# Optimization experiments

Measured on AMD Instinct MI355X. Metric: run time of the kernel, lower is better.

## Reference

```python
import jax, jax.numpy as jnp
import numpy as np

WS = 7      # window size
SHIFT = 3   # shift size
H = 56
W = 56
NH = 16     # num heads


def _layernorm(x, g, b):
    m = x.mean(-1, keepdims=True)
    v = x.var(-1, keepdims=True)
    return (x - m) / jnp.sqrt(v + 1e-5) * g + b


def setup_inputs() -> dict:
    key = jax.random.key(0)
    ks = jax.random.split(key, 8)
    B, C = 16, 512
    DH = 4 * C
    s = 0.02
    x = jax.random.normal(ks[0], (B, H * W, C), jnp.float32)

    # relative position index (matches torch buffer construction)
    coords = np.stack(np.meshgrid(np.arange(WS), np.arange(WS), indexing='ij')).reshape(2, -1)
    rel = (coords[:, :, None] - coords[:, None, :]).transpose(1, 2, 0).copy()
    rel[..., 0] += WS - 1
    rel[..., 1] += WS - 1
    rel[..., 0] *= 2 * WS - 1
    rpi = jnp.asarray(rel.sum(-1), jnp.int32)  # (49, 49)

    # shifted-window additive attention mask (nW, N, N)
    img = np.zeros((H, W))
    cnt = 0
    for hs in (slice(0, -WS), slice(-WS, -SHIFT), slice(-SHIFT, None)):
        for wsl in (slice(0, -WS), slice(-WS, -SHIFT), slice(-SHIFT, None)):
            img[hs, wsl] = cnt
            cnt += 1
    mw = img.reshape(H // WS, WS, W // WS, WS).transpose(0, 2, 1, 3).reshape(-1, WS * WS)
    diff = mw[:, None, :] - mw[:, :, None]  # == mw.unsqueeze(1) - mw.unsqueeze(2)
    attn_mask = jnp.asarray(np.where(diff != 0, -100.0, 0.0), jnp.float32)

    return {
        'x': x,
        'rpi': rpi,
        'attn_mask': attn_mask,
        'norm1_g': jnp.ones((C,), jnp.float32),
        'norm1_b': jnp.zeros((C,), jnp.float32),
        'qkv_w': jax.random.normal(ks[1], (3 * C, C), jnp.float32) * s,
        'qkv_b': jnp.zeros((3 * C,), jnp.float32),
        'proj_w': jax.random.normal(ks[2], (C, C), jnp.float32) * s,
        'proj_b': jnp.zeros((C,), jnp.float32),
        'rpb_table': jax.random.normal(ks[3], ((2 * WS - 1) ** 2, NH), jnp.float32) * s,
        'norm2_g': jnp.ones((C,), jnp.float32),
        'norm2_b': jnp.zeros((C,), jnp.float32),
        'mlp_w1': jax.random.normal(ks[4], (DH, C), jnp.float32) * s,
        'mlp_b1': jnp.zeros((DH,), jnp.float32),
        'mlp_w2': jax.random.normal(ks[5], (C, DH), jnp.float32) * s,
        'mlp_b2': jnp.zeros((C,), jnp.float32),
    }


def reference(x, rpi, attn_mask, norm1_g, norm1_b, qkv_w, qkv_b, proj_w, proj_b,
              rpb_table, norm2_g, norm2_b, mlp_w1, mlp_b1, mlp_w2, mlp_b2):
    B, L, C = x.shape
    N = WS * WS
    nW = (H // WS) * (W // WS)
    hd = C // NH

    # --- attention branch ---
    h = _layernorm(x, norm1_g, norm1_b).reshape(B, H, W, C)
    h = jnp.roll(h, (-SHIFT, -SHIFT), axis=(1, 2))
    # window partition -> (B*nW, N, C)
    xw = h.reshape(B, H // WS, WS, W // WS, WS, C).transpose(0, 1, 3, 2, 4, 5).reshape(B * nW, N, C)

    qkv = (xw @ qkv_w.T + qkv_b).reshape(B * nW, N, 3, NH, hd).transpose(2, 0, 3, 1, 4)
    q, k, v = qkv[0], qkv[1], qkv[2]  # (B*nW, NH, N, hd)
    attn = jnp.einsum('bhnd,bhmd->bhnm', q * (hd ** -0.5), k)
    rpb = rpb_table[rpi].transpose(2, 0, 1)  # (NH, N, N)
    attn = attn + rpb[None]
    attn = attn.reshape(B, nW, NH, N, N) + attn_mask[None, :, None]
    attn = jax.nn.softmax(attn.reshape(B * nW, NH, N, N), axis=-1)
    o = jnp.einsum('bhnm,bhmd->bhnd', attn, v).transpose(0, 2, 1, 3).reshape(B * nW, N, C)
    o = o @ proj_w.T + proj_b
    # window reverse + unshift
    o = o.reshape(B, H // WS, W // WS, WS, WS, C).transpose(0, 1, 3, 2, 4, 5).reshape(B, H, W, C)
    o = jnp.roll(o, (SHIFT, SHIFT), axis=(1, 2)).reshape(B, L, C)

    x = x + o
    # --- MLP branch ---
    h2 = _layernorm(x, norm2_g, norm2_b)
    m = jax.nn.gelu(h2 @ mlp_w1.T + mlp_b1, approximate=False)
    return x + (m @ mlp_w2.T + mlp_b2)
```

## Files before the change

### kernel.cpp

```cpp
#include <hip/hip_runtime.h>
#include <hip/hip_bf16.h>

typedef __attribute__((ext_vector_type(8))) short bf16x8_t;
typedef __attribute__((ext_vector_type(4))) float f32x4_t;

#define LD8(p) (*(const bf16x8_t*)(p))

__global__ __launch_bounds__(256) void k_cvt(const float* __restrict__ in,
                                             __hip_bfloat16* __restrict__ out, int n) {
  int i = blockIdx.x * 256 + threadIdx.x;
  if (i < n) out[i] = __float2bfloat16(in[i]);
}

__global__ __launch_bounds__(256) void k_cmb(const int* __restrict__ rpi,
                                             const float* __restrict__ tab,
                                             const float* __restrict__ mask,
                                             float* __restrict__ cmbp) {
  int idx = blockIdx.x * 256 + threadIdx.x;
  int jj = idx & 3, lane = (idx >> 2) & 63, tile = (idx >> 8) & 15;
  int h = (idx >> 12) & 15, w6 = idx >> 16;
  int r = (tile >> 2) * 16 + (lane >> 4) * 4 + jj;
  int c = (tile & 3) * 16 + (lane & 15);
  float v = -1e9f;
  if (r < 49 && c < 49) v = tab[rpi[r * 49 + c] * 16 + h] + mask[w6 * 2401 + r * 49 + c];
  cmbp[idx] = v;
}

template<int PERM>
__global__ __launch_bounds__(256) void k_ln(const float* __restrict__ in,
                                            const float* __restrict__ g,
                                            const float* __restrict__ bta,
                                            __hip_bfloat16* __restrict__ out) {
  int token = blockIdx.x;
  int t = threadIdx.x;
  const float2 v = ((const float2*)(in + (size_t)token * 512))[t];
  float s = v.x + v.y, sq = v.x * v.x + v.y * v.y;
  #pragma unroll
  for (int d = 1; d < 64; d <<= 1) { s += __shfl_xor(s, d); sq += __shfl_xor(sq, d); }
  __shared__ float ps[4], pq[4];
  int w = t >> 6;
  if ((t & 63) == 0) { ps[w] = s; pq[w] = sq; }
  __syncthreads();
  s  = ps[0] + ps[1] + ps[2] + ps[3];
  sq = pq[0] + pq[1] + pq[2] + pq[3];
  float mean = s * (1.f / 512.f);
  float inv = rsqrtf(sq * (1.f / 512.f) - mean * mean + 1e-5f);
  size_t dst;
  if (PERM) {
    int b = token / 3136, p = token - b * 3136;
    int i = p / 56, j = p - i * 56;
    int gi = (i + 53) % 56, gj = (j + 53) % 56;
    dst = ((size_t)(((b * 64) + (gi / 7) * 8 + (gj / 7)) * 49) + (gi % 7) * 7 + (gj % 7)) * 512;
  } else {
    dst = (size_t)token * 512;
  }
  int c = t * 2;
  out[dst + c]     = __float2bfloat16((v.x - mean) * inv * g[c] + bta[c]);
  out[dst + c + 1] = __float2bfloat16((v.y - mean) * inv * g[c + 1] + bta[c + 1]);
}

__global__ __launch_bounds__(256) void k_attn(const __hip_bfloat16* __restrict__ qkv,
                                              const float* __restrict__ cmbp,
                                              __hip_bfloat16* __restrict__ o) {
  __shared__ __align__(16) __hip_bfloat16 vt_all[4 * 32 * 72];
  __shared__ __align__(16) __hip_bfloat16 P_all[4 * 64 * 72];
  const int t = threadIdx.x, l = t & 63, w = t >> 6;
  const int bw = blockIdx.x;
  const int head = blockIdx.y * 4 + w;
  const int rr = l & 15, g = l >> 4;
  __hip_bfloat16* vt = vt_all + w * (32 * 72);
  __hip_bfloat16* P  = P_all  + w * (64 * 72);
  const __hip_bfloat16* base = qkv + (size_t)bw * 49 * 1536 + head * 32;
  const bf16x8_t zero8 = {};

  { int d = l >> 1, sg = (l & 1) * 8;
    *(bf16x8_t*)(vt + d * 72 + 48 + sg) = zero8; }
  __builtin_amdgcn_sched_barrier(0);
  #pragma unroll
  for (int it = 0; it < 4; ++it) {
    int idx = l + it * 64;
    if (idx < 196) {
      int j = idx >> 2, sg = (idx & 3) * 8;
      bf16x8_t vv = *(const bf16x8_t*)(base + 1024 + (size_t)j * 1536 + sg);
      #pragma unroll
      for (int s2 = 0; s2 < 8; ++s2) vt[(sg + s2) * 72 + j] = ((__hip_bfloat16*)&vv)[s2];
    }
  }
  bf16x8_t aq[4], bk[4];
  #pragma unroll
  for (int m = 0; m < 4; ++m) {
    int row = m * 16 + rr;
    aq[m] = (row < 49) ? *(const bf16x8_t*)(base + (size_t)row * 1536 + g * 8) : zero8;
    bk[m] = (row < 49) ? *(const bf16x8_t*)(base + 512 + (size_t)row * 1536 + g * 8) : zero8;
  }
  const float4* cp = (const float4*)(cmbp + (size_t)((bw & 63) * 16 + head) * 4096);
  f32x4_t S[4][4];
  #pragma unroll
  for (int tm = 0; tm < 4; ++tm)
    #pragma unroll
    for (int tn = 0; tn < 4; ++tn) {
      float4 cv = cp[(tm * 4 + tn) * 64 + l];
      f32x4_t c0 = { cv.x, cv.y, cv.z, cv.w };
      S[tm][tn] = __builtin_amdgcn_mfma_f32_16x16x32_bf16(aq[tm], bk[tn], c0, 0, 0, 0);
    }
  float sm[4][4];
  #pragma unroll
  for (int tm = 0; tm < 4; ++tm) {
    #pragma unroll
    for (int jj = 0; jj < 4; ++jj) {
      float v = fmaxf(fmaxf(S[tm][0][jj], S[tm][1][jj]), fmaxf(S[tm][2][jj], S[tm][3][jj]));
      v = fmaxf(v, __shfl_xor(v, 1));
      v = fmaxf(v, __shfl_xor(v, 2));
      v = fmaxf(v, __shfl_xor(v, 4));
      v = fmaxf(v, __shfl_xor(v, 8));
      float s = 0.f;
      #pragma unroll
      for (int tn = 0; tn < 4; ++tn) {
        float e = __expf(S[tm][tn][jj] - v);
        S[tm][tn][jj] = e;
        s += e;
      }
      s += __shfl_xor(s, 1); s += __shfl_xor(s, 2); s += __shfl_xor(s, 4); s += __shfl_xor(s, 8);
      sm[tm][jj] = s;
    }
  }
  #pragma unroll
  for (int tm = 0; tm < 4; ++tm)
    #pragma unroll
    for (int tn = 0; tn < 4; ++tn)
      #pragma unroll
      for (int jj = 0; jj < 4; ++jj)
        P[(tm * 16 + g * 4 + jj) * 72 + tn * 16 + rr] = __float2bfloat16(S[tm][tn][jj]);

  f32x4_t O[4][2] = {};
  #pragma unroll
  for (int ks = 0; ks < 2; ++ks) {
    bf16x8_t pa[4], vb[2];
    #pragma unroll
    for (int tm = 0; tm < 4; ++tm)
      pa[tm] = *(const bf16x8_t*)(P + (tm * 16 + rr) * 72 + ks * 32 + g * 8);
    #pragma unroll
    for (int tn = 0; tn < 2; ++tn)
      vb[tn] = *(const bf16x8_t*)(vt + (tn * 16 + rr) * 72 + ks * 32 + g * 8);
    #pragma unroll
    for (int tm = 0; tm < 4; ++tm)
      #pragma unroll
      for (int tn = 0; tn < 2; ++tn)
        O[tm][tn] = __builtin_amdgcn_mfma_f32_16x16x32_bf16(pa[tm], vb[tn], O[tm][tn], 0, 0, 0);
  }
  #pragma unroll
  for (int tm = 0; tm < 4; ++tm) {
    #pragma unroll
    for (int jj = 0; jj < 4; ++jj) {
      int r = tm * 16 + g * 4 + jj;
      if (r < 49) {
        float rcp = 1.f / sm[tm][jj];
        size_t ob = ((size_t)bw * 49 + r) * 512 + head * 32;
        o[ob + rr]      = __float2bfloat16(O[tm][0][jj] * rcp);
        o[ob + 16 + rr] = __float2bfloat16(O[tm][1][jj] * rcp);
      }
    }
  }
}

template<int EP>
__global__ __launch_bounds__(512, 2) void gemm256(const __hip_bfloat16* __restrict__ A,
                                                  const __hip_bfloat16* __restrict__ Bw,
                                                  int K, int Ncols, int nNB,
                                                  const float* __restrict__ bias,
                                                  __hip_bfloat16* __restrict__ obf,
                                                  const float* __restrict__ resid,
                                                  float* __restrict__ ofp) {
  __shared__ __align__(16) char LDS[131072];
  const int nwg = gridDim.x, orig = blockIdx.x;
  const int q8 = nwg >> 3, r8 = nwg & 7;
  const int xcd = orig & 7, lin = orig >> 3;
  const int wgid = (xcd < r8 ? xcd * (q8 + 1) : r8 * (q8 + 1) + (xcd - r8) * q8) + lin;
  const int bx = wgid / nNB, by = wgid - bx * nNB;
  const int m0 = bx * 256, n0 = by * 256;
  const int t = threadIdx.x, l = t & 63, w = t >> 6;
  const int wr = w >> 2, wc = w & 3;
  const int rr = l & 15, kq = l >> 4;
  const int lofs = rr * 64 + ((kq * 16) ^ ((rr & 8) << 2));

  int rs0, cs0, rs1, cs1;
  { int d = t * 16;        rs0 = (d >> 10) * 16 + ((d >> 6) & 15); cs0 = (d & 63) >> 1; }
  { int d = 8192 + t * 16; rs1 = (d >> 10) * 16 + ((d >> 6) & 15); cs1 = (d & 63) >> 1; }
  const __hip_bfloat16* gA0 = A  + (size_t)(m0 + rs0) * K + cs0;
  const __hip_bfloat16* gA1 = A  + (size_t)(m0 + rs1) * K + cs1;
  const __hip_bfloat16* gB0 = Bw + (size_t)(n0 + rs0) * K + cs0;
  const __hip_bfloat16* gB1 = Bw + (size_t)(n0 + rs1) * K + cs1;
  const int d0i = t * 16, d1i = 8192 + t * 16;
  const int wz0 = (d0i & ~63) | ((d0i & 63) ^ (((d0i >> 9) & 1) << 5));
  const int wz1 = (d1i & ~63) | ((d1i & 63) ^ (((d1i >> 9) & 1) << 5));

  bf16x8_t sa0, sa1, sb0, sb1;
  auto loadS = [&](int tile) {
    int c = tile * 32;
    sa0 = LD8(gA0 + c); sa1 = LD8(gA1 + c);
    sb0 = LD8(gB0 + c); sb1 = LD8(gB1 + c);
  };
  auto writeSA = [&](int tile) {
    char* d = LDS + (tile & 3) * 16384;
    *(bf16x8_t*)(d + wz0) = sa0; *(bf16x8_t*)(d + wz1) = sa1;
  };
  auto writeSB = [&](int tile) {
    char* d = LDS + 65536 + (tile & 3) * 16384;
    *(bf16x8_t*)(d + wz0) = sb0; *(bf16x8_t*)(d + wz1) = sb1;
  };

  f32x4_t acc[8][4] = {};

  const int NT = K >> 5;
  loadS(0); writeSA(0); writeSB(0);
  loadS(1); writeSA(1); writeSB(1);
  loadS(2); writeSA(2); writeSB(2);
  loadS(3);
  asm volatile("s_waitcnt lgkmcnt(0)" ::: "memory");
  __builtin_amdgcn_s_barrier();

  for (int kt = 0; kt < NT; ++kt) {
    const char* bA = LDS + (kt & 3) * 16384 + wr * 8192;
    const char* bB = LDS + 65536 + (kt & 3) * 16384 + wc * 4096;
    bf16x8_t ar[4], br[4];
    #pragma unroll
    for (int m = 0; m < 4; ++m) ar[m] = *(const bf16x8_t*)(bA + m * 1024 + lofs);
    #pragma unroll
    for (int n = 0; n < 4; ++n) br[n] = *(const bf16x8_t*)(bB + n * 1024 + lofs);
    if (kt + 3 < NT) writeSA(kt + 3);
    __builtin_amdgcn_s_barrier();
    asm volatile("s_waitcnt lgkmcnt(0)" ::: "memory");
    __builtin_amdgcn_sched_barrier(0);
    __builtin_amdgcn_s_setprio(1);
    #pragma unroll
    for (int m = 0; m < 4; ++m)
      #pragma unroll
      for (int n = 0; n < 4; ++n)
        acc[m][n] = __builtin_amdgcn_mfma_f32_16x16x32_bf16(ar[m], br[n], acc[m][n], 0, 0, 0);
    __builtin_amdgcn_s_setprio(0);
    __builtin_amdgcn_s_barrier();
    #pragma unroll
    for (int m = 0; m < 4; ++m) ar[m] = *(const bf16x8_t*)(bA + (4 + m) * 1024 + lofs);
    if (kt + 3 < NT) writeSB(kt + 3);
    if (kt + 4 < NT) loadS(kt + 4);
    __builtin_amdgcn_s_barrier();
    asm volatile("s_waitcnt lgkmcnt(0)" ::: "memory");
    __builtin_amdgcn_sched_barrier(0);
    __builtin_amdgcn_s_setprio(1);
    #pragma unroll
    for (int m = 0; m < 4; ++m)
      #pragma unroll
      for (int n = 0; n < 4; ++n)
        acc[4 + m][n] = __builtin_amdgcn_mfma_f32_16x16x32_bf16(ar[m], br[n], acc[4 + m][n], 0, 0, 0);
    __builtin_amdgcn_s_setprio(0);
    __builtin_amdgcn_s_barrier();
  }

  #pragma unroll
  for (int m = 0; m < 8; ++m) {
    #pragma unroll
    for (int n = 0; n < 4; ++n) {
      const int gcol = n0 + wc * 64 + n * 16 + rr;
      #pragma unroll
      for (int j = 0; j < 4; ++j) {
        const int grow = m0 + wr * 128 + m * 16 + kq * 4 + j;
        float v = acc[m][n][j] + bias[gcol];
        if (EP == 0) {
          if (gcol < 512) v *= 0.17677669529663687f;
          obf[(size_t)grow * Ncols + gcol] = __float2bfloat16(v);
        } else if (EP == 1) {
          int bw = grow / 49, nn = grow - bw * 49;
          int b = bw >> 6, wi = bw & 63;
          int hh = (wi >> 3) * 7 + nn / 7 + 3;  if (hh >= 56) hh -= 56;
          int ww2 = (wi & 7) * 7 + (nn % 7) + 3; if (ww2 >= 56) ww2 -= 56;
          size_t tok = (size_t)b * 3136 + hh * 56 + ww2;
          ofp[tok * 512 + gcol] = resid[tok * 512 + gcol] + v;
        } else if (EP == 2) {
          float u = 0.5f * v * (1.f + erff(v * 0.70710678118f));
          obf[(size_t)grow * Ncols + gcol] = __float2bfloat16(u);
        } else {
          ofp[(size_t)grow * 512 + gcol] += v;
        }
      }
    }
  }
}

extern "C" void kernel_launch(void* const* d_in, const int* in_sizes, int n_in,
                              void* d_out, int out_size, void* d_ws, size_t ws_size,
                              hipStream_t stream) {
  const float* x      = (const float*)d_in[0];
  const int*   rpi    = (const int*)  d_in[1];
  const float* amask  = (const float*)d_in[2];
  const float* n1g    = (const float*)d_in[3];
  const float* n1b    = (const float*)d_in[4];
  const float* qkv_w  = (const float*)d_in[5];
  const float* qkv_b  = (const float*)d_in[6];
  const float* proj_w = (const float*)d_in[7];
  const float* proj_b = (const float*)d_in[8];
  const float* rpb_t  = (const float*)d_in[9];
  const float* n2g    = (const float*)d_in[10];
  const float* n2b    = (const float*)d_in[11];
  const float* w1     = (const float*)d_in[12];
  const float* b1     = (const float*)d_in[13];
  const float* w2     = (const float*)d_in[14];
  const float* b2     = (const float*)d_in[15];
  float* out = (float*)d_out;

  char* ws = (char*)d_ws;
  const size_t M = 50176;
  const size_t szA = M * 2048 * 2;
  const size_t szB = M * 1536 * 2;
  const size_t offB = szA;
  const size_t offW = offB + szB;
  __hip_bfloat16* bufA = (__hip_bfloat16*)(ws);
  __hip_bfloat16* bufB = (__hip_bfloat16*)(ws + offB);
  __hip_bfloat16* wqkv  = (__hip_bfloat16*)(ws + offW);
  __hip_bfloat16* wproj = wqkv + 786432;
  __hip_bfloat16* wm1   = wproj + 262144;
  __hip_bfloat16* wm2   = wm1 + 1048576;
  float* cmbp = (float*)(ws + szA - (size_t)4194304 * 4);

  k_cvt<<<3072, 256, 0, stream>>>(qkv_w, wqkv, 786432);
  k_cvt<<<1024, 256, 0, stream>>>(proj_w, wproj, 262144);
  k_cvt<<<4096, 256, 0, stream>>>(w1, wm1, 1048576);
  k_cvt<<<4096, 256, 0, stream>>>(w2, wm2, 1048576);
  k_cmb<<<16384, 256, 0, stream>>>(rpi, rpb_t, amask, cmbp);

  k_ln<1><<<50176, 256, 0, stream>>>(x, n1g, n1b, bufA);
  gemm256<0><<<196 * 6, 512, 0, stream>>>(bufA, wqkv, 512, 1536, 6, qkv_b, bufB, nullptr, nullptr);
  k_attn<<<dim3(1024, 4), 256, 0, stream>>>(bufB, cmbp, bufA);
  gemm256<1><<<196 * 2, 512, 0, stream>>>(bufA, wproj, 512, 512, 2, proj_b, nullptr, x, out);
  k_ln<0><<<50176, 256, 0, stream>>>(out, n2g, n2b, bufB);
  gemm256<2><<<196 * 8, 512, 0, stream>>>(bufB, wm1, 512, 2048, 8, b1, bufA, nullptr, nullptr);
  gemm256<3><<<196 * 2, 512, 0, stream>>>(bufA, wm2, 2048, 512, 2, b2, nullptr, nullptr, out);
}
```

Before: 922.5 us.

## Load GEMM B operand directly from global into registers, shrink tile to 256x128

Rewrites the GEMM so the weight (B) operand is loaded straight from global memory into MFMA-layout registers instead of being staged through LDS. Only A is staged, in a 3-buffer LDS ring with ping-pong register sets. The output tile shrinks from 256x256 to 256x128 and the grids double to match. This cuts LDS traffic and footprint, but each wave now issues uncoalesced strided global loads for B, gets less reuse per tile, and launch bounds drop to one block per CU.

```diff
diff --git a/kernel.cpp b/kernel.cpp
--- a/kernel.cpp
+++ b/kernel.cpp
@@ -164,106 +164,98 @@
 }
 
 template<int EP>
-__global__ __launch_bounds__(512, 2) void gemm256(const __hip_bfloat16* __restrict__ A,
+__global__ __launch_bounds__(512, 1) void gemm_bd(const __hip_bfloat16* __restrict__ A,
                                                   const __hip_bfloat16* __restrict__ Bw,
                                                   int K, int Ncols, int nNB,
                                                   const float* __restrict__ bias,
                                                   __hip_bfloat16* __restrict__ obf,
                                                   const float* __restrict__ resid,
                                                   float* __restrict__ ofp) {
-  __shared__ __align__(16) char LDS[131072];
+  __shared__ __align__(16) char LDS[49152];
   const int nwg = gridDim.x, orig = blockIdx.x;
   const int q8 = nwg >> 3, r8 = nwg & 7;
   const int xcd = orig & 7, lin = orig >> 3;
   const int wgid = (xcd < r8 ? xcd * (q8 + 1) : r8 * (q8 + 1) + (xcd - r8) * q8) + lin;
   const int bx = wgid / nNB, by = wgid - bx * nNB;
-  const int m0 = bx * 256, n0 = by * 256;
+  const int m0 = bx * 256, n0 = by * 128;
   const int t = threadIdx.x, l = t & 63, w = t >> 6;
-  const int wr = w >> 2, wc = w & 3;
+  const int wr = w >> 1, wc = w & 1;
   const int rr = l & 15, kq = l >> 4;
   const int lofs = rr * 64 + ((kq * 16) ^ ((rr & 8) << 2));
 
   int rs0, cs0, rs1, cs1;
   { int d = t * 16;        rs0 = (d >> 10) * 16 + ((d >> 6) & 15); cs0 = (d & 63) >> 1; }
   { int d = 8192 + t * 16; rs1 = (d >> 10) * 16 + ((d >> 6) & 15); cs1 = (d & 63) >> 1; }
-  const __hip_bfloat16* gA0 = A  + (size_t)(m0 + rs0) * K + cs0;
-  const __hip_bfloat16* gA1 = A  + (size_t)(m0 + rs1) * K + cs1;
-  const __hip_bfloat16* gB0 = Bw + (size_t)(n0 + rs0) * K + cs0;
-  const __hip_bfloat16* gB1 = Bw + (size_t)(n0 + rs1) * K + cs1;
+  const __hip_bfloat16* gA0 = A + (size_t)(m0 + rs0) * K + cs0;
+  const __hip_bfloat16* gA1 = A + (size_t)(m0 + rs1) * K + cs1;
   const int d0i = t * 16, d1i = 8192 + t * 16;
   const int wz0 = (d0i & ~63) | ((d0i & 63) ^ (((d0i >> 9) & 1) << 5));
   const int wz1 = (d1i & ~63) | ((d1i & 63) ^ (((d1i >> 9) & 1) << 5));
 
-  bf16x8_t sa0, sa1, sb0, sb1;
-  auto loadS = [&](int tile) {
-    int c = tile * 32;
-    sa0 = LD8(gA0 + c); sa1 = LD8(gA1 + c);
-    sb0 = LD8(gB0 + c); sb1 = LD8(gB1 + c);
+  const __hip_bfloat16* gB = Bw + (size_t)(n0 + wc * 64 + rr) * K + kq * 8;
+  const size_t nstep = (size_t)16 * K;
+
+  bf16x8_t sE0, sE1, sO0, sO1;
+  auto loadE  = [&](int tile) { int c = tile * 32; sE0 = LD8(gA0 + c); sE1 = LD8(gA1 + c); };
+  auto loadO  = [&](int tile) { int c = tile * 32; sO0 = LD8(gA0 + c); sO1 = LD8(gA1 + c); };
+  auto writeE = [&](int tile) { char* d = LDS + (tile % 3) * 16384;
+                                *(bf16x8_t*)(d + wz0) = sE0; *(bf16x8_t*)(d + wz1) = sE1; };
+  auto writeO = [&](int tile) { char* d = LDS + (tile % 3) * 16384;
+                                *(bf16x8_t*)(d + wz0) = sO0; *(bf16x8_t*)(d + wz1) = sO1; };
+  auto rdA = [&](bf16x8_t (&a)[4], int tile) {
+    const char* b = LDS + (tile % 3) * 16384 + wr * 4096;
+    #pragma unroll
+    for (int m = 0; m < 4; ++m) a[m] = *(const bf16x8_t*)(b + m * 1024 + lofs);
   };
-  auto writeSA = [&](int tile) {
-    char* d = LDS + (tile & 3) * 16384;
-    *(bf16x8_t*)(d + wz0) = sa0; *(bf16x8_t*)(d + wz1) = sa1;
+  auto ldB = [&](bf16x8_t (&bv)[4], int tile) {
+    const __hip_bfloat16* p = gB + tile * 32;
+    #pragma unroll
+    for (int n = 0; n < 4; ++n) bv[n] = LD8(p + n * nstep);
   };
-  auto writeSB = [&](int tile) {
-    char* d = LDS + 65536 + (tile & 3) * 16384;
-    *(bf16x8_t*)(d + wz0) = sb0; *(bf16x8_t*)(d + wz1) = sb1;
+
+  f32x4_t acc[4][4] = {};
+  auto mma = [&](bf16x8_t (&a)[4], bf16x8_t (&bv)[4]) {
+    __builtin_amdgcn_s_setprio(1);
+    #pragma unroll
+    for (int m = 0; m < 4; ++m)
+      #pragma unroll
+      for (int n = 0; n < 4; ++n)
+        acc[m][n] = __builtin_amdgcn_mfma_f32_16x16x32_bf16(a[m], bv[n], acc[m][n], 0, 0, 0);
+    __builtin_amdgcn_s_setprio(0);
   };
 
-  f32x4_t acc[8][4] = {};
-
   const int NT = K >> 5;
-  loadS(0); writeSA(0); writeSB(0);
-  loadS(1); writeSA(1); writeSB(1);
-  loadS(2); writeSA(2); writeSB(2);
-  loadS(3);
+  bf16x8_t a0[4], b0[4], a1[4], b1[4];
+
+  loadE(0); loadO(1); writeE(0); writeO(1); loadE(2); loadO(3);
   asm volatile("s_waitcnt lgkmcnt(0)" ::: "memory");
   __builtin_amdgcn_s_barrier();
-
-  for (int kt = 0; kt < NT; ++kt) {
-    const char* bA = LDS + (kt & 3) * 16384 + wr * 8192;
-    const char* bB = LDS + 65536 + (kt & 3) * 16384 + wc * 4096;
-    bf16x8_t ar[4], br[4];
-    #pragma unroll
-    for (int m = 0; m < 4; ++m) ar[m] = *(const bf16x8_t*)(bA + m * 1024 + lofs);
-    #pragma unroll
-    for (int n = 0; n < 4; ++n) br[n] = *(const bf16x8_t*)(bB + n * 1024 + lofs);
-    if (kt + 3 < NT) writeSA(kt + 3);
+  rdA(a0, 0); ldB(b0, 0);
+
+  for (int kt = 0; kt < NT; kt += 2) {
+    ldB(b1, kt + 1); rdA(a1, kt + 1);
+    if (kt + 2 < NT) writeE(kt + 2);
+    if (kt + 4 < NT) loadE(kt + 4);
+    mma(a0, b0);
+    asm volatile("s_waitcnt lgkmcnt(0)" ::: "memory");
     __builtin_amdgcn_s_barrier();
+    const int k2 = kt + 1;
+    if (k2 + 1 < NT) { ldB(b0, k2 + 1); rdA(a0, k2 + 1); }
+    if (k2 + 2 < NT) writeO(k2 + 2);
+    if (k2 + 4 < NT) loadO(k2 + 4);
+    mma(a1, b1);
     asm volatile("s_waitcnt lgkmcnt(0)" ::: "memory");
-    __builtin_amdgcn_sched_barrier(0);
-    __builtin_amdgcn_s_setprio(1);
-    #pragma unroll
-    for (int m = 0; m < 4; ++m)
-      #pragma unroll
-      for (int n = 0; n < 4; ++n)
-        acc[m][n] = __builtin_amdgcn_mfma_f32_16x16x32_bf16(ar[m], br[n], acc[m][n], 0, 0, 0);
-    __builtin_amdgcn_s_setprio(0);
     __builtin_amdgcn_s_barrier();
-    #pragma unroll
-    for (int m = 0; m < 4; ++m) ar[m] = *(const bf16x8_t*)(bA + (4 + m) * 1024 + lofs);
-    if (kt + 3 < NT) writeSB(kt + 3);
-    if (kt + 4 < NT) loadS(kt + 4);
-    __builtin_amdgcn_s_barrier();
-    asm volatile("s_waitcnt lgkmcnt(0)" ::: "memory");
-    __builtin_amdgcn_sched_barrier(0);
-    __builtin_amdgcn_s_setprio(1);
-    #pragma unroll
-    for (int m = 0; m < 4; ++m)
-      #pragma unroll
-      for (int n = 0; n < 4; ++n)
-        acc[4 + m][n] = __builtin_amdgcn_mfma_f32_16x16x32_bf16(ar[m], br[n], acc[4 + m][n], 0, 0, 0);
-    __builtin_amdgcn_s_setprio(0);
-    __builtin_amdgcn_s_barrier();
-  }
-
-  #pragma unroll
-  for (int m = 0; m < 8; ++m) {
+  }
+
+  #pragma unroll
+  for (int m = 0; m < 4; ++m) {
     #pragma unroll
     for (int n = 0; n < 4; ++n) {
       const int gcol = n0 + wc * 64 + n * 16 + rr;
       #pragma unroll
       for (int j = 0; j < 4; ++j) {
-        const int grow = m0 + wr * 128 + m * 16 + kq * 4 + j;
+        const int grow = m0 + wr * 64 + m * 16 + kq * 4 + j;
         float v = acc[m][n][j] + bias[gcol];
         if (EP == 0) {
           if (gcol < 512) v *= 0.17677669529663687f;
@@ -328,10 +320,10 @@
   k_cmb<<<16384, 256, 0, stream>>>(rpi, rpb_t, amask, cmbp);
 
   k_ln<1><<<50176, 256, 0, stream>>>(x, n1g, n1b, bufA);
-  gemm256<0><<<196 * 6, 512, 0, stream>>>(bufA, wqkv, 512, 1536, 6, qkv_b, bufB, nullptr, nullptr);
+  gemm_bd<0><<<196 * 12, 512, 0, stream>>>(bufA, wqkv, 512, 1536, 12, qkv_b, bufB, nullptr, nullptr);
   k_attn<<<dim3(1024, 4), 256, 0, stream>>>(bufB, cmbp, bufA);
-  gemm256<1><<<196 * 2, 512, 0, stream>>>(bufA, wproj, 512, 512, 2, proj_b, nullptr, x, out);
+  gemm_bd<1><<<196 * 4, 512, 0, stream>>>(bufA, wproj, 512, 512, 4, proj_b, nullptr, x, out);
   k_ln<0><<<50176, 256, 0, stream>>>(out, n2g, n2b, bufB);
-  gemm256<2><<<196 * 8, 512, 0, stream>>>(bufB, wm1, 512, 2048, 8, b1, bufA, nullptr, nullptr);
-  gemm256<3><<<196 * 2, 512, 0, stream>>>(bufA, wm2, 2048, 512, 2, b2, nullptr, nullptr, out);
-}
+  gemm_bd<2><<<196 * 16, 512, 0, stream>>>(bufB, wm1, 512, 2048, 16, b1, bufA, nullptr, nullptr);
+  gemm_bd<3><<<196 * 4, 512, 0, stream>>>(bufA, wm2, 2048, 512, 4, b2, nullptr, nullptr, out);
+}
```

New measurement: 1.251 ms. 35.6% more time.
